# Kernel tuning notes

Hardware: AMD Instinct MI355X
Metric: run time of the kernel (lower is better)

## Reference

```python
import jax, jax.numpy as jnp
import numpy as np
import math

N = 128
SIZE = N * N
K = 16
ORDER = 2
DIM = 2

def _exponents(order):
    # 2D Taylor monomial exponents (a,b) with 1 <= a+b <= order
    return [(a, d - a) for d in range(1, order + 1) for a in range(d, -1, -1)]

EXPS = _exponents(ORDER)
NUM_DERIV = len(EXPS)  # n(n+3)/2 = 5 for order 2, matches TP_layer.num_derivatives


def setup_inputs() -> dict:
    key = jax.random.key(0)
    k0, k1, k2, k3, k4 = jax.random.split(key, 5)
    B = 32
    x = jax.random.normal(k0, (B, SIZE), dtype=jnp.float32)
    points = jax.random.uniform(k1, (B, SIZE, DIM), dtype=jnp.float32)
    edge_index = jax.random.randint(k2, (B, SIZE * K), 0, SIZE)
    dist = jax.random.uniform(k3, (B, SIZE, K), dtype=jnp.float32)
    dt = jnp.float32(0.01)
    # PDELinear weight: shape (1, 1, num_derivatives), uniform(-0.1, 0.1)
    weight = jax.random.uniform(k4, (1, 1, NUM_DERIV), dtype=jnp.float32,
                                minval=-0.1, maxval=0.1)
    return {"x": x, "points": points, "edge_index": edge_index,
            "dt": dt, "dist": dist, "weight": weight}


def _solve_derivatives(points, knn_points, values, knn_values, dist):
    # points: [B,S,2]  knn_points: [B,S,K,2]  values: [B,S]  knn_values: [B,S,K]
    off = knn_points - points[:, :, None, :]          # [B,S,K,2]
    dx, dy = off[..., 0], off[..., 1]
    cols = [(dx ** a) * (dy ** b) / (math.factorial(a) * math.factorial(b))
            for (a, b) in EXPS]
    A = jnp.stack(cols, axis=-1)                      # [B,S,K,D] Taylor design matrix
    rhs = knn_values - values[..., None]              # [B,S,K]
    Aw = A * dist[..., None]                          # weighted least squares
    bw = rhs * dist
    AtA = jnp.einsum('bski,bskj->bsij', Aw, Aw)       # [B,S,D,D]
    Atb = jnp.einsum('bski,bsk->bsi', Aw, bw)         # [B,S,D]
    ridge = jnp.float32(1e-6) * jnp.eye(NUM_DERIV, dtype=A.dtype)
    deriv = jnp.linalg.solve(AtA + ridge, Atb[..., None])[..., 0]  # [B,S,D]
    return deriv


def reference(x, points, edge_index, dt, dist, weight):
    B = x.shape[0]
    values = x.reshape(B, SIZE)
    # per-batch kNN gather (vectorized index_select)
    knn_p = jnp.take_along_axis(points, edge_index[..., None], axis=1)
    knn_p = knn_p.reshape(B, SIZE, K, DIM)
    knn_v = jnp.take_along_axis(values[..., None], edge_index[..., None], axis=1)
    knn_v = knn_v.reshape(B, SIZE, K)
    deriv = _solve_derivatives(points, knn_p, values, knn_v, dist)
    deriv = jax.lax.stop_gradient(deriv)              # torch.no_grad in original
    du = jnp.sum(deriv * weight[0], axis=-1)          # PDELinear broadcast + sum -> [B,S]
    return x + dt * du
```

## Files before the change

kernel.cpp:

```cpp
#include <hip/hip_runtime.h>

#define TPL_SIZE 16384
#define TPL_K 16
#define TPL_ND 5
#define TPL_BLK 512
#define TPL_PTS 4
#define TPL_SPAN (TPL_BLK * TPL_PTS)
#define TPL_BPB (TPL_SIZE / TPL_SPAN)
#define TPL_ITER (TPL_SIZE / TPL_BLK)
#define TPL_NXCD 8

__global__ __launch_bounds__(TPL_BLK, 2) void tp_lds_kernel(
    const float* __restrict__ x,
    const float* __restrict__ points,
    const int*   __restrict__ edge_index,
    const float* __restrict__ dtp,
    const float* __restrict__ dist,
    const float* __restrict__ weight,
    float* __restrict__ out)
{
    extern __shared__ uint2 lds_pv[];

    const int tid = threadIdx.x;
    const int blk = blockIdx.x;

    const int xcd   = blk & (TPL_NXCD - 1);
    const int batch = xcd * 4 + (blk >> 6);
    const int chunk = (blk >> 3) & (TPL_BPB - 1);

    const size_t base = (size_t)batch * TPL_SIZE + chunk * TPL_SPAN;

    int4   ci[4];
    float4 cw[4];
    {
        const int4*   ei = reinterpret_cast<const int4*>(edge_index + (base + tid) * TPL_K);
        const float4* dw = reinterpret_cast<const float4*>(dist      + (base + tid) * TPL_K);
        ci[0] = ei[0]; ci[1] = ei[1]; ci[2] = ei[2]; ci[3] = ei[3];
        cw[0] = dw[0]; cw[1] = dw[1]; cw[2] = dw[2]; cw[3] = dw[3];
    }

    const float2* pb = reinterpret_cast<const float2*>(points) + (size_t)batch * TPL_SIZE;
    const float*  xb = x + (size_t)batch * TPL_SIZE;

    #pragma unroll
    for (int k = 0; k < TPL_ITER; ++k) {
        int i = tid + k * TPL_BLK;
        float2 p = pb[i];
        float  v = xb[i];
        unsigned ux = (unsigned)(p.x * 65536.0f);
        unsigned uy = (unsigned)(p.y * 65536.0f);
        if (ux > 65535u) ux = 65535u;
        if (uy > 65535u) uy = 65535u;
        uint2 e;
        e.x = ux | (uy << 16);
        e.y = __float_as_uint(v);
        lds_pv[i] = e;
    }
    __syncthreads();

    const float wt0 = weight[0], wt1 = weight[1], wt2 = weight[2],
                wt3 = weight[3], wt4 = weight[4];
    const float dtv = dtp[0];

    #pragma unroll
    for (int p = 0; p < TPL_PTS; ++p) {
        int4   ni[4];
        float4 nw[4];
        if (p < TPL_PTS - 1) {
            const size_t rown = base + (p + 1) * TPL_BLK + tid;
            const int4*   ei = reinterpret_cast<const int4*>(edge_index + rown * TPL_K);
            const float4* dw = reinterpret_cast<const float4*>(dist      + rown * TPL_K);
            ni[0] = ei[0]; ni[1] = ei[1]; ni[2] = ei[2]; ni[3] = ei[3];
            nw[0] = dw[0]; nw[1] = dw[1]; nw[2] = dw[2]; nw[3] = dw[3];
        }

        const int    s   = chunk * TPL_SPAN + p * TPL_BLK + tid;
        const size_t row = base + p * TPL_BLK + tid;

        uint2 se = lds_pv[s];
        unsigned sx = se.x & 0xffffu;
        unsigned sy = se.x >> 16;
        float    sv = __uint_as_float(se.y);

        int ids[TPL_K] = {ci[0].x, ci[0].y, ci[0].z, ci[0].w,
                          ci[1].x, ci[1].y, ci[1].z, ci[1].w,
                          ci[2].x, ci[2].y, ci[2].z, ci[2].w,
                          ci[3].x, ci[3].y, ci[3].z, ci[3].w};
        float wgt[TPL_K] = {cw[0].x, cw[0].y, cw[0].z, cw[0].w,
                            cw[1].x, cw[1].y, cw[1].z, cw[1].w,
                            cw[2].x, cw[2].y, cw[2].z, cw[2].w,
                            cw[3].x, cw[3].y, cw[3].z, cw[3].w};

        uint2 nb[TPL_K];
        #pragma unroll
        for (int t = 0; t < TPL_K; ++t) nb[t] = lds_pv[ids[t] & (TPL_SIZE - 1)];

        float ata[15], atb[TPL_ND];
        #pragma unroll
        for (int i = 0; i < 15; ++i) ata[i] = 0.0f;
        #pragma unroll
        for (int i = 0; i < TPL_ND; ++i) atb[i] = 0.0f;

        #pragma unroll
        for (int t = 0; t < TPL_K; ++t) {
            float w = wgt[t];
            int dxi = (int)(nb[t].x & 0xffffu) - (int)sx;
            int dyi = (int)(nb[t].x >> 16)     - (int)sy;
            float dx = (float)dxi * 0x1p-16f;
            float dy = (float)dyi * 0x1p-16f;
            float nv = __uint_as_float(nb[t].y);
            float a[TPL_ND];
            a[0] = dx * w;
            a[1] = dy * w;
            a[2] = 0.5f * dx * dx * w;
            a[3] = dx * dy * w;
            a[4] = 0.5f * dy * dy * w;
            float bwv = (nv - sv) * w;
            int c = 0;
            #pragma unroll
            for (int i = 0; i < TPL_ND; ++i) {
                #pragma unroll
                for (int j = i; j < TPL_ND; ++j) ata[c++] += a[i] * a[j];
                atb[i] += a[i] * bwv;
            }
        }

        float M[TPL_ND][TPL_ND], r[TPL_ND], pinv[TPL_ND];
        {
            int c = 0;
            #pragma unroll
            for (int i = 0; i < TPL_ND; ++i) {
                #pragma unroll
                for (int j = i; j < TPL_ND; ++j) { M[i][j] = ata[c]; M[j][i] = ata[c]; ++c; }
                r[i] = atb[i];
                M[i][i] += 1e-6f;
            }
        }
        #pragma unroll
        for (int i = 0; i < TPL_ND; ++i) {
            float inv = __builtin_amdgcn_rcpf(M[i][i]);
            pinv[i] = inv;
            #pragma unroll
            for (int j = i + 1; j < TPL_ND; ++j) {
                float f = M[j][i] * inv;
                #pragma unroll
                for (int cc = i + 1; cc < TPL_ND; ++cc) M[j][cc] -= f * M[i][cc];
                r[j] -= f * r[i];
            }
        }
        float sol[TPL_ND];
        #pragma unroll
        for (int i = TPL_ND - 1; i >= 0; --i) {
            float sv2 = r[i];
            #pragma unroll
            for (int cc = i + 1; cc < TPL_ND; ++cc) sv2 -= M[i][cc] * sol[cc];
            sol[i] = sv2 * pinv[i];
        }

        float du = sol[0] * wt0 + sol[1] * wt1 + sol[2] * wt2
                 + sol[3] * wt3 + sol[4] * wt4;
        out[row] = sv + dtv * du;

        if (p < TPL_PTS - 1) {
            #pragma unroll
            for (int q = 0; q < 4; ++q) { ci[q] = ni[q]; cw[q] = nw[q]; }
        }
    }
}

extern "C" void kernel_launch(void* const* d_in, const int* in_sizes, int n_in,
                              void* d_out, int out_size, void* d_ws, size_t ws_size,
                              hipStream_t stream) {
    const float* x          = (const float*)d_in[0];
    const float* points     = (const float*)d_in[1];
    const int*   edge_index = (const int*)d_in[2];
    const float* dtp        = (const float*)d_in[3];
    const float* dist       = (const float*)d_in[4];
    const float* weight     = (const float*)d_in[5];
    float* out = (float*)d_out;

    int total = out_size;
    int grid  = total / TPL_SPAN;
    size_t lds_bytes = (size_t)TPL_SIZE * sizeof(uint2);

    tp_lds_kernel<<<grid, TPL_BLK, lds_bytes, stream>>>(
        x, points, edge_index, dtp, dist, weight, out);
}
```

Baseline: 21.14 us.

## Double block size to 1024 threads, vectorize LDS fill, move next-row prefetch

New measurement: 53.62 us. 2.54x slower.

```diff
diff --git a/kernel.cpp b/kernel.cpp
--- a/kernel.cpp
+++ b/kernel.cpp
@@ -3,14 +3,15 @@
 #define TPL_SIZE 16384
 #define TPL_K 16
 #define TPL_ND 5
-#define TPL_BLK 512
-#define TPL_PTS 4
+#define TPL_BLK 1024
+#define TPL_PTS 2
 #define TPL_SPAN (TPL_BLK * TPL_PTS)
 #define TPL_BPB (TPL_SIZE / TPL_SPAN)
-#define TPL_ITER (TPL_SIZE / TPL_BLK)
 #define TPL_NXCD 8
 
-__global__ __launch_bounds__(TPL_BLK, 2) void tp_lds_kernel(
+__global__ __launch_bounds__(TPL_BLK, 4)
+__attribute__((amdgpu_waves_per_eu(4, 4)))
+void tp_lds_kernel(
     const float* __restrict__ x,
     const float* __restrict__ points,
     const int*   __restrict__ edge_index,
@@ -39,22 +40,30 @@
         cw[0] = dw[0]; cw[1] = dw[1]; cw[2] = dw[2]; cw[3] = dw[3];
     }
 
-    const float2* pb = reinterpret_cast<const float2*>(points) + (size_t)batch * TPL_SIZE;
-    const float*  xb = x + (size_t)batch * TPL_SIZE;
-
-    #pragma unroll
-    for (int k = 0; k < TPL_ITER; ++k) {
-        int i = tid + k * TPL_BLK;
-        float2 p = pb[i];
-        float  v = xb[i];
-        unsigned ux = (unsigned)(p.x * 65536.0f);
-        unsigned uy = (unsigned)(p.y * 65536.0f);
-        if (ux > 65535u) ux = 65535u;
-        if (uy > 65535u) uy = 65535u;
-        uint2 e;
-        e.x = ux | (uy << 16);
-        e.y = __float_as_uint(v);
-        lds_pv[i] = e;
+    {
+        const float4* pb4 = reinterpret_cast<const float4*>(points + (size_t)batch * TPL_SIZE * 2);
+        const float2* xb2 = reinterpret_cast<const float2*>(x + (size_t)batch * TPL_SIZE);
+        uint4* lds4 = reinterpret_cast<uint4*>(lds_pv);
+        #pragma unroll
+        for (int k = 0; k < TPL_SIZE / (2 * TPL_BLK); ++k) {
+            int g = k * TPL_BLK + tid;
+            float4 pp = pb4[g];
+            float2 xv = xb2[g];
+            unsigned ux0 = (unsigned)(pp.x * 65536.0f);
+            unsigned uy0 = (unsigned)(pp.y * 65536.0f);
+            unsigned ux1 = (unsigned)(pp.z * 65536.0f);
+            unsigned uy1 = (unsigned)(pp.w * 65536.0f);
+            if (ux0 > 65535u) ux0 = 65535u;
+            if (uy0 > 65535u) uy0 = 65535u;
+            if (ux1 > 65535u) ux1 = 65535u;
+            if (uy1 > 65535u) uy1 = 65535u;
+            uint4 wv;
+            wv.x = ux0 | (uy0 << 16);
+            wv.y = __float_as_uint(xv.x);
+            wv.z = ux1 | (uy1 << 16);
+            wv.w = __float_as_uint(xv.y);
+            lds4[g] = wv;
+        }
     }
     __syncthreads();
 
@@ -64,16 +73,6 @@
 
     #pragma unroll
     for (int p = 0; p < TPL_PTS; ++p) {
-        int4   ni[4];
-        float4 nw[4];
-        if (p < TPL_PTS - 1) {
-            const size_t rown = base + (p + 1) * TPL_BLK + tid;
-            const int4*   ei = reinterpret_cast<const int4*>(edge_index + rown * TPL_K);
-            const float4* dw = reinterpret_cast<const float4*>(dist      + rown * TPL_K);
-            ni[0] = ei[0]; ni[1] = ei[1]; ni[2] = ei[2]; ni[3] = ei[3];
-            nw[0] = dw[0]; nw[1] = dw[1]; nw[2] = dw[2]; nw[3] = dw[3];
-        }
-
         const int    s   = chunk * TPL_SPAN + p * TPL_BLK + tid;
         const size_t row = base + p * TPL_BLK + tid;
 
@@ -94,6 +93,14 @@
         uint2 nb[TPL_K];
         #pragma unroll
         for (int t = 0; t < TPL_K; ++t) nb[t] = lds_pv[ids[t] & (TPL_SIZE - 1)];
+
+        if (p < TPL_PTS - 1) {
+            const size_t rown = base + (p + 1) * TPL_BLK + tid;
+            const int4*   ei = reinterpret_cast<const int4*>(edge_index + rown * TPL_K);
+            const float4* dw = reinterpret_cast<const float4*>(dist      + rown * TPL_K);
+            #pragma unroll
+            for (int q = 0; q < 4; ++q) { ci[q] = ei[q]; cw[q] = dw[q]; }
+        }
 
         float ata[15], atb[TPL_ND];
         #pragma unroll
@@ -160,11 +167,6 @@
         float du = sol[0] * wt0 + sol[1] * wt1 + sol[2] * wt2
                  + sol[3] * wt3 + sol[4] * wt4;
         out[row] = sv + dtv * du;
-
-        if (p < TPL_PTS - 1) {
-            #pragma unroll
-            for (int q = 0; q < 4; ++q) { ci[q] = ni[q]; cw[q] = nw[q]; }
-        }
     }
 }
 
```
